# Performance work log

Measured on AMD Instinct MI355X. Metric: run time of the kernel, lower is better.

The kernel has to match this reference:

```python
import jax, jax.numpy as jnp
import numpy as np

H = 56; W = 56; WS = 7; NW = WS * WS  # 49 tokens per window
HEADS = 8; DIM = 256; HIDDEN = 4 * DIM
SHIFT = NW // 2  # gilbert shift = 24 (shift_size > 0)
SCALE = (DIM // HEADS) ** -0.5
EPS = 1e-5


def _sgn(v):
    return -1 if v < 0 else 1 if v > 0 else 0


def _generate2d(x, y, ax, ay, bx, by, result):
    w = abs(ax + ay); h = abs(bx + by)
    dax, day = _sgn(ax), _sgn(ay); dbx, dby = _sgn(bx), _sgn(by)
    if h == 1 or w == 1:
        if h == 1:
            for _ in range(w):
                result.append((x, y)); x, y = x + dax, y + day
        elif w == 1:
            for _ in range(h):
                result.append((x, y)); x, y = x + dbx, y + dby
        return
    ax2, ay2 = ax // 2, ay // 2; bx2, by2 = bx // 2, by // 2
    w2 = abs(ax2 + ay2); h2 = abs(bx2 + by2)
    if 2 * w > 3 * h:
        if w2 % 2 and w > 2:
            ax2, ay2 = ax2 + dax, ay2 + day
        _generate2d(x, y, ax2, ay2, bx, by, result)
        _generate2d(x + ax2, y + ay2, ax - ax2, ay - ay2, bx, by, result)
    else:
        if h2 % 2 and h > 2:
            bx2, by2 = bx2 + dbx, by2 + dby
        _generate2d(x, y, bx2, by2, ax2, ay2, result)
        _generate2d(x + bx2, y + by2, ax, ay, bx - bx2, by - by2, result)
        _generate2d(x + (ax - dax) + (bx2 - dbx), y + (ay - day) + (by2 - dby),
                    -bx2, -by2, -(ax - ax2), -(ay - ay2), result)


def _gilbert2d(width, height):
    result = []
    if width >= height:
        _generate2d(0, 0, width, 0, 0, height, result)
    else:
        _generate2d(0, 0, 0, height, width, 0, result)
    return result


def _make_rel_index():
    # reverse_map[idx] = (y, x) for gilbert position idx
    path = _gilbert2d(W, H)
    rev = np.zeros((H * W, 2), dtype=np.int64)
    for i, (px, py) in enumerate(path[:H * W]):
        rev[i, 0] = py; rev[i, 1] = px
    pos = np.roll(rev, SHIFT, axis=0)  # shifted block: roll positions by ws^2//2
    n_windows = (H * W) // NW
    pos = pos[:n_windows * NW].reshape(n_windows, NW, 2)
    dh = pos[:, :, 0][:, :, None] - pos[:, :, 0][:, None, :] + (H - 1)
    dw = pos[:, :, 1][:, :, None] - pos[:, :, 1][:, None, :] + (W - 1)
    return (dh * (2 * W - 1) + dw).astype(np.int32)  # (nW, 49, 49)


def setup_inputs() -> dict:
    key = jax.random.key(0)
    ks = jax.random.split(key, 8)
    B, L, C = 32, H * W, DIM
    return {
        "x": jax.random.normal(ks[0], (B, L, C), jnp.float32),
        "qkv_w": jax.random.normal(ks[1], (C, 3 * C), jnp.float32) * 0.02,
        "qkv_b": jnp.zeros((3 * C,), jnp.float32),
        "proj_w": jax.random.normal(ks[2], (C, C), jnp.float32) * 0.02,
        "proj_b": jnp.zeros((C,), jnp.float32),
        "bias_table": jax.random.normal(ks[3], ((2 * H - 1) * (2 * W - 1), HEADS), jnp.float32) * 0.02,
        "norm1_w": jnp.ones((C,), jnp.float32),
        "norm1_b": jnp.zeros((C,), jnp.float32),
        "norm2_w": jnp.ones((C,), jnp.float32),
        "norm2_b": jnp.zeros((C,), jnp.float32),
        "fc1_w": jax.random.normal(ks[4], (C, HIDDEN), jnp.float32) * 0.02,
        "fc1_b": jnp.zeros((HIDDEN,), jnp.float32),
        "fc2_w": jax.random.normal(ks[5], (HIDDEN, C), jnp.float32) * 0.02,
        "fc2_b": jnp.zeros((C,), jnp.float32),
        "rel_index": jnp.asarray(_make_rel_index()),
    }


def _layernorm(x, w, b):
    mu = jnp.mean(x, axis=-1, keepdims=True)
    var = jnp.mean(jnp.square(x - mu), axis=-1, keepdims=True)
    return (x - mu) * jax.lax.rsqrt(var + EPS) * w + b


def reference(x, qkv_w, qkv_b, proj_w, proj_b, bias_table,
              norm1_w, norm1_b, norm2_w, norm2_b,
              fc1_w, fc1_b, fc2_w, fc2_b, rel_index):
    B, L, C = x.shape
    n_win = L // NW
    hd = C // HEADS

    shortcut = x
    h = _layernorm(x, norm1_w, norm1_b)
    # gilbert forward shift along the curve, then window partition
    h = jnp.roll(h, SHIFT, axis=1)
    hw = h.reshape(B * n_win, NW, C)

    qkv = (hw @ qkv_w + qkv_b).reshape(B * n_win, NW, 3, HEADS, hd)
    qkv = jnp.transpose(qkv, (2, 0, 3, 1, 4))  # (3, B*nW, heads, N, hd)
    q, k, v = qkv[0] * SCALE, qkv[1], qkv[2]

    attn = jnp.einsum('bhnd,bhmd->bhnm', q, k)  # (B*nW, heads, 49, 49)
    bias = jnp.transpose(bias_table[rel_index], (0, 3, 1, 2))  # (nW, heads, 49, 49)
    attn = attn.reshape(B, n_win, HEADS, NW, NW) + bias[None]
    attn = jax.nn.softmax(attn, axis=-1).reshape(B * n_win, HEADS, NW, NW)

    out = jnp.einsum('bhnm,bhmd->bhnd', attn, v)
    out = jnp.transpose(out, (0, 2, 1, 3)).reshape(B * n_win, NW, C)
    out = out @ proj_w + proj_b

    # window merge + gilbert reverse shift
    out = out.reshape(B, L, C)
    out = jnp.roll(out, -SHIFT, axis=1)

    x = shortcut + out
    h2 = _layernorm(x, norm2_w, norm2_b)
    h2 = jax.nn.gelu(h2 @ fc1_w + fc1_b, approximate=False) @ fc2_w + fc2_b
    return x + h2
```

## Files before the change

### kernel.cpp

```cpp
#include <hip/hip_runtime.h>
#include <math.h>

typedef unsigned short u16;
typedef __attribute__((ext_vector_type(8))) short bfrag;
typedef __attribute__((ext_vector_type(4))) float f32x4;
typedef __attribute__((ext_vector_type(4))) unsigned short us4;

#define B_SZ 32
#define L_SZ 3136
#define C_SZ 256
#define NHEADS 8
#define HID_SZ 1024
#define NW 49
#define NWIN 64
#define SHIFT 24
#define M_SZ (B_SZ * L_SZ)
#define SCALEF 0.17677669529663687f

__device__ __forceinline__ float bf2f(u16 u) {
  union { unsigned int i; float f; } v; v.i = ((unsigned)u) << 16; return v.f;
}
__device__ __forceinline__ u16 f2bf(float f) {
  union { unsigned int i; float f; } v; v.f = f;
  return (u16)((v.i + 0x7fffu + ((v.i >> 16) & 1u)) >> 16);
}
__device__ __forceinline__ void gload_lds16(const u16* g, u16* l) {
  __builtin_amdgcn_global_load_lds(
      (const __attribute__((address_space(1))) unsigned int*)g,
      (__attribute__((address_space(3))) unsigned int*)l, 16, 0, 0);
}

__global__ void transpose_kernel(const float* __restrict__ in, u16* __restrict__ out,
                                 int K, int N) {
  const int idx = blockIdx.x * 256 + threadIdx.x;
  if (idx >= K * N) return;
  const int n = idx / K;
  const int k = idx - n * K;
  out[idx] = f2bf(in[(size_t)k * N + n]);
}

__global__ void bias_kernel(const float* __restrict__ tab, const int* __restrict__ rel,
                            float* __restrict__ bm) {
  const int idx = blockIdx.x * 256 + threadIdx.x;
  const int tot = NWIN * NHEADS * NW * NW;
  if (idx >= tot) return;
  const int w = idx / (NHEADS * NW * NW);
  const int r = idx - w * (NHEADS * NW * NW);
  const int h = r / (NW * NW);
  const int ij = r - h * (NW * NW);
  bm[idx] = tab[(size_t)rel[w * NW * NW + ij] * NHEADS + h];
}

__global__ __launch_bounds__(256) void ln1_kernel(
    const float* __restrict__ x, const float* __restrict__ w,
    const float* __restrict__ b, u16* __restrict__ out) {
  const int wv = threadIdx.x >> 6;
  const int lane = threadIdx.x & 63;
  const int row0 = blockIdx.x * 16 + wv * 4;
  float4 u[4];
#pragma unroll
  for (int r = 0; r < 4; ++r)
    u[r] = *((const float4*)x + (size_t)(row0 + r) * 64 + lane);
  float s[4], sq[4];
#pragma unroll
  for (int r = 0; r < 4; ++r) {
    s[r]  = u[r].x + u[r].y + u[r].z + u[r].w;
    sq[r] = u[r].x * u[r].x + u[r].y * u[r].y + u[r].z * u[r].z + u[r].w * u[r].w;
  }
#pragma unroll
  for (int d = 1; d < 64; d <<= 1)
#pragma unroll
    for (int r = 0; r < 4; ++r) {
      s[r] += __shfl_xor(s[r], d); sq[r] += __shfl_xor(sq[r], d);
    }
  float wv4[4], bv4[4];
#pragma unroll
  for (int j = 0; j < 4; ++j) { wv4[j] = w[lane * 4 + j]; bv4[j] = b[lane * 4 + j]; }
#pragma unroll
  for (int r = 0; r < 4; ++r) {
    const int row = row0 + r;
    const float mu = s[r] * (1.0f / C_SZ);
    const float rs = rsqrtf(sq[r] * (1.0f / C_SZ) - mu * mu + 1e-5f);
    const int bb = row / L_SZ;
    int l2 = row - bb * L_SZ + SHIFT;
    if (l2 >= L_SZ) l2 -= L_SZ;
    const float vv[4] = {u[r].x, u[r].y, u[r].z, u[r].w};
    us4 ov;
#pragma unroll
    for (int j = 0; j < 4; ++j) ov[j] = f2bf((vv[j] - mu) * rs * wv4[j] + bv4[j]);
    *(us4*)(out + ((size_t)bb * L_SZ + l2) * C_SZ + lane * 4) = ov;
  }
}

__global__ __launch_bounds__(256) void ln2_kernel(
    const u16* __restrict__ x, const float* __restrict__ w,
    const float* __restrict__ b, u16* __restrict__ out) {
  const int wv = threadIdx.x >> 6;
  const int lane = threadIdx.x & 63;
  const int row0 = blockIdx.x * 16 + wv * 4;
  us4 u[4];
#pragma unroll
  for (int r = 0; r < 4; ++r)
    u[r] = *(const us4*)(x + (size_t)(row0 + r) * C_SZ + lane * 4);
  float v[4][4], s[4], sq[4];
#pragma unroll
  for (int r = 0; r < 4; ++r) {
    s[r] = 0.f; sq[r] = 0.f;
#pragma unroll
    for (int j = 0; j < 4; ++j) {
      v[r][j] = bf2f(u[r][j]); s[r] += v[r][j]; sq[r] += v[r][j] * v[r][j];
    }
  }
#pragma unroll
  for (int d = 1; d < 64; d <<= 1)
#pragma unroll
    for (int r = 0; r < 4; ++r) {
      s[r] += __shfl_xor(s[r], d); sq[r] += __shfl_xor(sq[r], d);
    }
  float wv4[4], bv4[4];
#pragma unroll
  for (int j = 0; j < 4; ++j) { wv4[j] = w[lane * 4 + j]; bv4[j] = b[lane * 4 + j]; }
#pragma unroll
  for (int r = 0; r < 4; ++r) {
    const float mu = s[r] * (1.0f / C_SZ);
    const float rs = rsqrtf(sq[r] * (1.0f / C_SZ) - mu * mu + 1e-5f);
    us4 ov;
#pragma unroll
    for (int j = 0; j < 4; ++j) ov[j] = f2bf((v[r][j] - mu) * rs * wv4[j] + bv4[j]);
    *(us4*)(out + (size_t)(row0 + r) * C_SZ + lane * 4) = ov;
  }
}

#define BM 128
#define BN 128
#define BKT 64

template <int MODE>
__global__ __launch_bounds__(256, 4) void gemm_kernel(
    const u16* __restrict__ A, const u16* __restrict__ Bt,
    const float* __restrict__ bias, int N, int K, void* __restrict__ Cout,
    const float* __restrict__ resx, const u16* __restrict__ resb2) {
  __shared__ u16 Als[BM * BKT];
  __shared__ u16 Bls[BN * BKT];
  const int nbx = N / BN;
  const int per = gridDim.x >> 3;
  const int lin = (blockIdx.x & 7) * per + (blockIdx.x >> 3);
  const int by = lin / nbx;
  const int bx = lin - by * nbx;
  const int m0 = by * BM;
  const int n0 = bx * BN;

  const int tid = threadIdx.x;
  const int lane = tid & 63;
  const int lr = lane & 15;
  const int lg = lane >> 4;
  const int wid = tid >> 6;
  const int wm = (wid >> 1) * 64;
  const int wn = (wid & 1) * 64;

  const int grow = lane >> 3;
  const int gch = (lane & 7) ^ grow;

  const f32x4 fzero = {0.f, 0.f, 0.f, 0.f};
  f32x4 acc[4][4];
#pragma unroll
  for (int i = 0; i < 4; ++i)
#pragma unroll
    for (int j = 0; j < 4; ++j) acc[i][j] = fzero;

  const u16* Agl = A + (size_t)m0 * K + gch * 8;
  const u16* Bgl = Bt + (size_t)n0 * K + gch * 8;

  for (int k0 = 0; k0 < K; k0 += BKT) {
#pragma unroll
    for (int g = 0; g < 4; ++g) {
      const int rbase = wid * 32 + g * 8;
      gload_lds16(Agl + (size_t)(rbase + grow) * K + k0, Als + rbase * 64);
      gload_lds16(Bgl + (size_t)(rbase + grow) * K + k0, Bls + rbase * 64);
    }
    __syncthreads();
#pragma unroll
    for (int s = 0; s < 2; ++s) {
      const int kg = s * 4 + lg;
      bfrag af[4], bfv[4];
#pragma unroll
      for (int m = 0; m < 4; ++m) {
        const int r = wm + m * 16 + lr;
        af[m] = *(const bfrag*)(Als + r * 64 + ((kg ^ (r & 7)) * 8));
      }
#pragma unroll
      for (int n = 0; n < 4; ++n) {
        const int r = wn + n * 16 + lr;
        bfv[n] = *(const bfrag*)(Bls + r * 64 + ((kg ^ (r & 7)) * 8));
      }
#pragma unroll
      for (int m = 0; m < 4; ++m)
#pragma unroll
        for (int n = 0; n < 4; ++n)
          acc[m][n] = __builtin_amdgcn_mfma_f32_16x16x32_bf16(af[m], bfv[n],
                                                              acc[m][n], 0, 0, 0);
    }
    __syncthreads();
  }

  float bv4[4];
#pragma unroll
  for (int n = 0; n < 4; ++n) bv4[n] = bias[n0 + wn + n * 16 + lr];

#pragma unroll
  for (int m = 0; m < 4; ++m) {
#pragma unroll
    for (int i = 0; i < 4; ++i) {
      const int row = m0 + wm + m * 16 + lg * 4 + i;
      if (MODE == 1) {
        const int bb = row / L_SZ;
        int l2 = row - bb * L_SZ - SHIFT;
        if (l2 < 0) l2 += L_SZ;
        const size_t orow = (size_t)bb * L_SZ + l2;
#pragma unroll
        for (int n = 0; n < 4; ++n) {
          const int col = n0 + wn + n * 16 + lr;
          ((u16*)Cout)[orow * N + col] =
              f2bf(resx[orow * N + col] + acc[m][n][i] + bv4[n]);
        }
      } else if (MODE == 2) {
#pragma unroll
        for (int n = 0; n < 4; ++n) {
          const int col = n0 + wn + n * 16 + lr;
          float v = acc[m][n][i] + bv4[n];
          const float t2 = 2.0f * v * (0.7978845608f + 0.0356774081f * v * v);
          v = v / (1.0f + __expf(-t2));
          ((u16*)Cout)[(size_t)row * N + col] = f2bf(v);
        }
      } else if (MODE == 3) {
#pragma unroll
        for (int n = 0; n < 4; ++n) {
          const int col = n0 + wn + n * 16 + lr;
          ((float*)Cout)[(size_t)row * N + col] =
              acc[m][n][i] + bv4[n] + bf2f(resb2[(size_t)row * N + col]);
        }
      } else {
#pragma unroll
        for (int n = 0; n < 4; ++n) {
          const int col = n0 + wn + n * 16 + lr;
          ((u16*)Cout)[(size_t)row * N + col] = f2bf(acc[m][n][i] + bv4[n]);
        }
      }
    }
  }
}

__global__ __launch_bounds__(256) void attn_kernel(const u16* __restrict__ qkv,
                                                   const float* __restrict__ bm,
                                                   u16* __restrict__ out, int widx0) {
  __shared__ u16 Pls[4][64 * 72];
  __shared__ u16 Vls[4][64 * 32];
  const int wl = blockIdx.x >> 1;
  const int half = blockIdx.x & 1;
  const int w = (widx0 + wl) & (NWIN - 1);
  const int wv = threadIdx.x >> 6;
  const int lane = threadIdx.x & 63;
  const int lr = lane & 15;
  const int lg = lane >> 4;
  const size_t base = (size_t)wl * NW;
  u16* P = Pls[wv];
  u16* Vl = Vls[wv];
  const f32x4 fzero = {0.f, 0.f, 0.f, 0.f};
  const int h = half * 4 + wv;

#pragma unroll
  for (int g = 0; g < 4; ++g) {
    int row = g * 16 + (lane >> 2);
    if (row > NW - 1) row = NW - 1;
    const int sc = (lane & 3) ^ ((row ^ (row >> 2)) & 3);
    gload_lds16(qkv + (base + row) * 768 + 512 + h * 32 + sc * 8, Vl + g * 512);
  }

  bfrag qf[4], kf[4];
#pragma unroll
  for (int m = 0; m < 4; ++m) {
    int r = m * 16 + lr; if (r > NW - 1) r = NW - 1;
    qf[m] = *(const bfrag*)(qkv + (base + r) * 768 + h * 32 + lg * 8);
    kf[m] = *(const bfrag*)(qkv + (base + r) * 768 + 256 + h * 32 + lg * 8);
  }
  f32x4 s[4][4];
#pragma unroll
  for (int m = 0; m < 4; ++m)
#pragma unroll
    for (int n = 0; n < 4; ++n)
      s[m][n] = __builtin_amdgcn_mfma_f32_16x16x32_bf16(qf[m], kf[n], fzero, 0, 0, 0);

  const float* bh = bm + (size_t)(w * NHEADS + h) * (NW * NW);
#pragma unroll
  for (int m = 0; m < 4; ++m) {
#pragma unroll
    for (int i = 0; i < 4; ++i) {
      const int row = m * 16 + lg * 4 + i;
      const int brow = row > NW - 1 ? NW - 1 : row;
      float vals[4];
#pragma unroll
      for (int n = 0; n < 4; ++n) {
        const int c = n * 16 + lr;
        vals[n] = (c < NW) ? (s[m][n][i] * SCALEF + bh[brow * NW + c]) : -1e30f;
      }
      float mx = fmaxf(fmaxf(vals[0], vals[1]), fmaxf(vals[2], vals[3]));
#pragma unroll
      for (int d = 1; d < 16; d <<= 1) mx = fmaxf(mx, __shfl_xor(mx, d));
      float sum = 0.f;
#pragma unroll
      for (int n = 0; n < 4; ++n) { vals[n] = __expf(vals[n] - mx); sum += vals[n]; }
#pragma unroll
      for (int d = 1; d < 16; d <<= 1) sum += __shfl_xor(sum, d);
      const float inv = 1.0f / sum;
#pragma unroll
      for (int n = 0; n < 4; ++n)
        P[row * 72 + n * 16 + lr] = f2bf(vals[n] * inv);
    }
  }
  asm volatile("s_waitcnt vmcnt(0)" ::: "memory");
  f32x4 o[4][2];
#pragma unroll
  for (int m = 0; m < 4; ++m) { o[m][0] = fzero; o[m][1] = fzero; }
#pragma unroll
  for (int s2 = 0; s2 < 2; ++s2) {
    bfrag pf[4], vf[2];
#pragma unroll
    for (int m = 0; m < 4; ++m)
      pf[m] = *(const bfrag*)(P + (m * 16 + lr) * 72 + s2 * 32 + lg * 8);
#pragma unroll
    for (int n = 0; n < 2; ++n) {
      const int d = n * 16 + lr;
      const int cd = d >> 3;
#pragma unroll
      for (int i = 0; i < 8; ++i) {
        const int kk = s2 * 32 + lg * 8 + i;
        const int slot = cd ^ ((kk ^ (kk >> 2)) & 3);
        vf[n][i] = *(const short*)(Vl + kk * 32 + slot * 8 + (d & 7));
      }
    }
#pragma unroll
    for (int m = 0; m < 4; ++m)
#pragma unroll
      for (int n = 0; n < 2; ++n)
        o[m][n] = __builtin_amdgcn_mfma_f32_16x16x32_bf16(pf[m], vf[n],
                                                          o[m][n], 0, 0, 0);
  }
#pragma unroll
  for (int m = 0; m < 4; ++m)
#pragma unroll
    for (int i = 0; i < 4; ++i) {
      const int row = m * 16 + lg * 4 + i;
      if (row < NW) {
#pragma unroll
        for (int n = 0; n < 2; ++n)
          out[(base + row) * C_SZ + h * 32 + n * 16 + lr] = f2bf(o[m][n][i]);
      }
    }
}

extern "C" void kernel_launch(void* const* d_in, const int* in_sizes, int n_in,
                              void* d_out, int out_size, void* d_ws, size_t ws_size,
                              hipStream_t stream) {
  (void)in_sizes; (void)n_in; (void)out_size;
  const float* x     = (const float*)d_in[0];
  const float* qkvw  = (const float*)d_in[1];
  const float* qkvb  = (const float*)d_in[2];
  const float* projw = (const float*)d_in[3];
  const float* projb = (const float*)d_in[4];
  const float* btab  = (const float*)d_in[5];
  const float* n1w   = (const float*)d_in[6];
  const float* n1b   = (const float*)d_in[7];
  const float* n2w   = (const float*)d_in[8];
  const float* n2b   = (const float*)d_in[9];
  const float* fc1w  = (const float*)d_in[10];
  const float* fc1b  = (const float*)d_in[11];
  const float* fc2w  = (const float*)d_in[12];
  const float* fc2b  = (const float*)d_in[13];
  const int* rel     = (const int*)d_in[14];

  char* ws = (char*)d_ws;
  size_t off = 0;
  auto alloc = [&](size_t bytes) -> char* {
    char* p = ws + off; off += (bytes + 255) & ~(size_t)255; return p;
  };
  u16* qkvwT   = (u16*)alloc((size_t)768 * 256 * 2);
  u16* projwT  = (u16*)alloc((size_t)256 * 256 * 2);
  u16* fc1wT   = (u16*)alloc((size_t)1024 * 256 * 2);
  u16* fc2wT   = (u16*)alloc((size_t)256 * 1024 * 2);
  float* biasm = (float*)alloc((size_t)NWIN * NHEADS * NW * NW * 4);
  u16* bufh    = (u16*)alloc((size_t)M_SZ * C_SZ * 2);
  u16* x2b     = (u16*)alloc((size_t)M_SZ * C_SZ * 2);

  const size_t scr_chunk = (size_t)(M_SZ / 2) * HID_SZ * 2;
  const int nch = (ws_size >= off + scr_chunk) ? 2 : 4;
  const int mch = M_SZ / nch;
  const int wch = (B_SZ * NWIN) / nch;
  char* tail = ws + off;
  u16* qkvbuf   = (u16*)tail;
  u16* scratch2 = (u16*)tail;

  transpose_kernel<<<(256 * 768 + 255) / 256, 256, 0, stream>>>(qkvw, qkvwT, 256, 768);
  transpose_kernel<<<(256 * 256 + 255) / 256, 256, 0, stream>>>(projw, projwT, 256, 256);
  transpose_kernel<<<(256 * 1024 + 255) / 256, 256, 0, stream>>>(fc1w, fc1wT, 256, 1024);
  transpose_kernel<<<(1024 * 256 + 255) / 256, 256, 0, stream>>>(fc2w, fc2wT, 1024, 256);
  bias_kernel<<<(NWIN * NHEADS * NW * NW + 255) / 256, 256, 0, stream>>>(btab, rel, biasm);

  ln1_kernel<<<M_SZ / 16, 256, 0, stream>>>(x, n1w, n1b, bufh);

  for (int c = 0; c < nch; ++c) {
    const size_t roff = (size_t)c * mch;
    gemm_kernel<0><<<(768 / BN) * (mch / BM), 256, 0, stream>>>(
        bufh + roff * C_SZ, qkvwT, qkvb, 768, 256, qkvbuf, nullptr, nullptr);
    attn_kernel<<<wch * 2, 256, 0, stream>>>(qkvbuf, biasm, bufh + roff * C_SZ,
                                             c * wch);
  }

  gemm_kernel<1><<<(256 / BN) * (M_SZ / BM), 256, 0, stream>>>(
      bufh, projwT, projb, 256, 256, x2b, x, nullptr);

  for (int q = 0; q < nch; ++q) {
    const size_t roff = (size_t)q * mch;
    ln2_kernel<<<mch / 16, 256, 0, stream>>>(x2b + roff * C_SZ, n2w, n2b,
                                             bufh + roff * C_SZ);
    gemm_kernel<2><<<(HID_SZ / BN) * (mch / BM), 256, 0, stream>>>(
        bufh + roff * C_SZ, fc1wT, fc1b, 1024, 256, scratch2, nullptr, nullptr);
    gemm_kernel<3><<<(256 / BN) * (mch / BM), 256, 0, stream>>>(
        scratch2, fc2wT, fc2b, 256, 1024, (float*)d_out + roff * C_SZ,
        nullptr, x2b + roff * C_SZ);
  }
}
```

Before: 464.7 us.

## Fuse projection GEMM, residual add and LayerNorm2 into one full-row kernel

```diff
diff --git a/kernel.cpp b/kernel.cpp
--- a/kernel.cpp
+++ b/kernel.cpp
@@ -92,45 +92,6 @@
   }
 }
 
-__global__ __launch_bounds__(256) void ln2_kernel(
-    const u16* __restrict__ x, const float* __restrict__ w,
-    const float* __restrict__ b, u16* __restrict__ out) {
-  const int wv = threadIdx.x >> 6;
-  const int lane = threadIdx.x & 63;
-  const int row0 = blockIdx.x * 16 + wv * 4;
-  us4 u[4];
-#pragma unroll
-  for (int r = 0; r < 4; ++r)
-    u[r] = *(const us4*)(x + (size_t)(row0 + r) * C_SZ + lane * 4);
-  float v[4][4], s[4], sq[4];
-#pragma unroll
-  for (int r = 0; r < 4; ++r) {
-    s[r] = 0.f; sq[r] = 0.f;
-#pragma unroll
-    for (int j = 0; j < 4; ++j) {
-      v[r][j] = bf2f(u[r][j]); s[r] += v[r][j]; sq[r] += v[r][j] * v[r][j];
-    }
-  }
-#pragma unroll
-  for (int d = 1; d < 64; d <<= 1)
-#pragma unroll
-    for (int r = 0; r < 4; ++r) {
-      s[r] += __shfl_xor(s[r], d); sq[r] += __shfl_xor(sq[r], d);
-    }
-  float wv4[4], bv4[4];
-#pragma unroll
-  for (int j = 0; j < 4; ++j) { wv4[j] = w[lane * 4 + j]; bv4[j] = b[lane * 4 + j]; }
-#pragma unroll
-  for (int r = 0; r < 4; ++r) {
-    const float mu = s[r] * (1.0f / C_SZ);
-    const float rs = rsqrtf(sq[r] * (1.0f / C_SZ) - mu * mu + 1e-5f);
-    us4 ov;
-#pragma unroll
-    for (int j = 0; j < 4; ++j) ov[j] = f2bf((v[r][j] - mu) * rs * wv4[j] + bv4[j]);
-    *(us4*)(out + (size_t)(row0 + r) * C_SZ + lane * 4) = ov;
-  }
-}
-
 #define BM 128
 #define BN 128
 #define BKT 64
@@ -139,7 +100,7 @@
 __global__ __launch_bounds__(256, 4) void gemm_kernel(
     const u16* __restrict__ A, const u16* __restrict__ Bt,
     const float* __restrict__ bias, int N, int K, void* __restrict__ Cout,
-    const float* __restrict__ resx, const u16* __restrict__ resb2) {
+    const u16* __restrict__ resb2) {
   __shared__ u16 Als[BM * BKT];
   __shared__ u16 Bls[BN * BKT];
   const int nbx = N / BN;
@@ -212,18 +173,7 @@
 #pragma unroll
     for (int i = 0; i < 4; ++i) {
       const int row = m0 + wm + m * 16 + lg * 4 + i;
-      if (MODE == 1) {
-        const int bb = row / L_SZ;
-        int l2 = row - bb * L_SZ - SHIFT;
-        if (l2 < 0) l2 += L_SZ;
-        const size_t orow = (size_t)bb * L_SZ + l2;
-#pragma unroll
-        for (int n = 0; n < 4; ++n) {
-          const int col = n0 + wn + n * 16 + lr;
-          ((u16*)Cout)[orow * N + col] =
-              f2bf(resx[orow * N + col] + acc[m][n][i] + bv4[n]);
-        }
-      } else if (MODE == 2) {
+      if (MODE == 2) {
 #pragma unroll
         for (int n = 0; n < 4; ++n) {
           const int col = n0 + wn + n * 16 + lr;
@@ -245,6 +195,99 @@
           const int col = n0 + wn + n * 16 + lr;
           ((u16*)Cout)[(size_t)row * N + col] = f2bf(acc[m][n][i] + bv4[n]);
         }
+      }
+    }
+  }
+}
+
+__global__ __launch_bounds__(256, 2) void projln_kernel(
+    const u16* __restrict__ A, const u16* __restrict__ Bt,
+    const float* __restrict__ bias, const float* __restrict__ x,
+    const float* __restrict__ n2w, const float* __restrict__ n2b,
+    u16* __restrict__ x2b, u16* __restrict__ h2) {
+  __shared__ u16 Als[128 * 64];
+  __shared__ u16 Bls[256 * 64];
+  const int per = gridDim.x >> 3;
+  const int by = (blockIdx.x & 7) * per + (blockIdx.x >> 3);
+  const int m0 = by * 128;
+  const int tid = threadIdx.x;
+  const int lane = tid & 63;
+  const int lr = lane & 15;
+  const int lg = lane >> 4;
+  const int wid = tid >> 6;
+  const int wm = wid * 32;
+  const int grow = lane >> 3;
+  const int gch = (lane & 7) ^ grow;
+  const f32x4 fzero = {0.f, 0.f, 0.f, 0.f};
+  f32x4 acc[2][16];
+#pragma unroll
+  for (int m = 0; m < 2; ++m)
+#pragma unroll
+    for (int n = 0; n < 16; ++n) acc[m][n] = fzero;
+
+  const u16* Agl = A + (size_t)m0 * 256 + gch * 8;
+  const u16* Bgl = Bt + gch * 8;
+
+  for (int k0 = 0; k0 < 256; k0 += 64) {
+#pragma unroll
+    for (int g = 0; g < 4; ++g) {
+      const int rb = wid * 32 + g * 8;
+      gload_lds16(Agl + (size_t)(rb + grow) * 256 + k0, Als + rb * 64);
+    }
+#pragma unroll
+    for (int g = 0; g < 8; ++g) {
+      const int rb = wid * 64 + g * 8;
+      gload_lds16(Bgl + (size_t)(rb + grow) * 256 + k0, Bls + rb * 64);
+    }
+    __syncthreads();
+#pragma unroll
+    for (int s = 0; s < 2; ++s) {
+      const int kg = s * 4 + lg;
+      bfrag af[2];
+#pragma unroll
+      for (int m = 0; m < 2; ++m) {
+        const int r = wm + m * 16 + lr;
+        af[m] = *(const bfrag*)(Als + r * 64 + ((kg ^ (r & 7)) * 8));
+      }
+#pragma unroll
+      for (int n = 0; n < 16; ++n) {
+        const int r = n * 16 + lr;
+        const bfrag bv = *(const bfrag*)(Bls + r * 64 + ((kg ^ (r & 7)) * 8));
+#pragma unroll
+        for (int m = 0; m < 2; ++m)
+          acc[m][n] = __builtin_amdgcn_mfma_f32_16x16x32_bf16(af[m], bv,
+                                                              acc[m][n], 0, 0, 0);
+      }
+    }
+    __syncthreads();
+  }
+
+#pragma unroll
+  for (int m = 0; m < 2; ++m) {
+#pragma unroll
+    for (int i = 0; i < 4; ++i) {
+      const int row = m0 + wm + m * 16 + lg * 4 + i;
+      const int bb = row / L_SZ;
+      int l2 = row - bb * L_SZ - SHIFT;
+      if (l2 < 0) l2 += L_SZ;
+      const size_t orow = (size_t)bb * L_SZ + l2;
+      float v[16]; float s = 0.f, sq = 0.f;
+#pragma unroll
+      for (int n = 0; n < 16; ++n) {
+        const int col = n * 16 + lr;
+        v[n] = acc[m][n][i] + bias[col] + x[orow * 256 + col];
+        s += v[n]; sq += v[n] * v[n];
+      }
+#pragma unroll
+      for (int d = 1; d < 16; d <<= 1) { s += __shfl_xor(s, d); sq += __shfl_xor(sq, d); }
+      const float mu = s * (1.0f / 256.0f);
+      const float rs = rsqrtf(sq * (1.0f / 256.0f) - mu * mu + 1e-5f);
+#pragma unroll
+      for (int n = 0; n < 16; ++n) {
+        const int col = n * 16 + lr;
+        const size_t idx = orow * 256 + col;
+        x2b[idx] = f2bf(v[n]);
+        h2[idx] = f2bf((v[n] - mu) * rs * n2w[col] + n2b[col]);
       }
     }
   }
@@ -390,6 +433,7 @@
   float* biasm = (float*)alloc((size_t)NWIN * NHEADS * NW * NW * 4);
   u16* bufh    = (u16*)alloc((size_t)M_SZ * C_SZ * 2);
   u16* x2b     = (u16*)alloc((size_t)M_SZ * C_SZ * 2);
+  u16* h2buf   = (u16*)alloc((size_t)M_SZ * C_SZ * 2);
 
   const size_t scr_chunk = (size_t)(M_SZ / 2) * HID_SZ * 2;
   const int nch = (ws_size >= off + scr_chunk) ? 2 : 4;
@@ -410,22 +454,20 @@
   for (int c = 0; c < nch; ++c) {
     const size_t roff = (size_t)c * mch;
     gemm_kernel<0><<<(768 / BN) * (mch / BM), 256, 0, stream>>>(
-        bufh + roff * C_SZ, qkvwT, qkvb, 768, 256, qkvbuf, nullptr, nullptr);
+        bufh + roff * C_SZ, qkvwT, qkvb, 768, 256, qkvbuf, nullptr);
     attn_kernel<<<wch * 2, 256, 0, stream>>>(qkvbuf, biasm, bufh + roff * C_SZ,
                                              c * wch);
   }
 
-  gemm_kernel<1><<<(256 / BN) * (M_SZ / BM), 256, 0, stream>>>(
-      bufh, projwT, projb, 256, 256, x2b, x, nullptr);
+  projln_kernel<<<M_SZ / 128, 256, 0, stream>>>(bufh, projwT, projb, x,
+                                                n2w, n2b, x2b, h2buf);
 
   for (int q = 0; q < nch; ++q) {
     const size_t roff = (size_t)q * mch;
-    ln2_kernel<<<mch / 16, 256, 0, stream>>>(x2b + roff * C_SZ, n2w, n2b,
-                                             bufh + roff * C_SZ);
     gemm_kernel<2><<<(HID_SZ / BN) * (mch / BM), 256, 0, stream>>>(
-        bufh + roff * C_SZ, fc1wT, fc1b, 1024, 256, scratch2, nullptr, nullptr);
+        h2buf + roff * C_SZ, fc1wT, fc1b, 1024, 256, scratch2, nullptr);
     gemm_kernel<3><<<(256 / BN) * (mch / BM), 256, 0, stream>>>(
         scratch2, fc2wT, fc2b, 256, 1024, (float*)d_out + roff * C_SZ,
-        nullptr, x2b + roff * C_SZ);
-  }
-}
+        x2b + roff * C_SZ);
+  }
+}
```

Result: slower. 588.1 us (+26.6%).
